# Kernel tuning notes

Measured on AMD Instinct MI355X. Metric: run time of the kernel, lower is better.

Reference implementation:

```python
import jax, jax.numpy as jnp
import numpy as np

DIM = 1024
HEADS = 16
DIM_HEAD = 64
INNER = HEADS * DIM_HEAD
SCALE = DIM_HEAD ** -0.5


def setup_inputs() -> dict:
    key = jax.random.key(0)
    ks = jax.random.split(key, 9)
    B, N = 4, 4096
    x = jax.random.normal(ks[0], (B, N, DIM), dtype=jnp.float32)
    mask = jnp.ones((B, N), dtype=bool)
    s = 0.02
    W_qkv = jax.random.normal(ks[1], (DIM, INNER * 3), dtype=jnp.float32) * s
    w_q = jax.random.normal(ks[2], (DIM_HEAD,), dtype=jnp.float32) * s
    w_k = jax.random.normal(ks[3], (DIM_HEAD,), dtype=jnp.float32) * s
    W_r = jax.random.normal(ks[4], (DIM_HEAD, DIM_HEAD), dtype=jnp.float32) * s
    b_r = jnp.zeros((DIM_HEAD,), dtype=jnp.float32)
    W_out = jax.random.normal(ks[5], (INNER, DIM), dtype=jnp.float32) * s
    b_out = jnp.zeros((DIM,), dtype=jnp.float32)
    return {"x": x, "mask": mask, "W_qkv": W_qkv, "w_q": w_q, "w_k": w_k,
            "W_r": W_r, "b_r": b_r, "W_out": W_out, "b_out": b_out}


def reference(x, mask, W_qkv, w_q, w_k, W_r, b_r, W_out, b_out):
    B, N, D = x.shape
    h, dh = HEADS, DIM_HEAD
    mask_value = -jnp.finfo(x.dtype).max

    qkv = x @ W_qkv                                  # [B,N,3*inner]
    q, k, v = jnp.split(qkv, 3, axis=-1)
    tohead = lambda t: t.reshape(B, N, h, dh).transpose(0, 2, 1, 3)  # b h n d
    q, k, v = tohead(q), tohead(k), tohead(v)
    m = mask[:, None, :]                             # b 1 n

    # global query via softmax-pooled per-token logits
    q_logits = jnp.einsum('bhnd,d->bhn', q, w_q) * SCALE
    q_attn = jax.nn.softmax(jnp.where(m, q_logits, mask_value), axis=-1)
    global_q = jnp.einsum('bhn,bhnd->bhd', q_attn, q)[:, :, None, :]  # b h 1 d

    k = k * global_q
    k_logits = jnp.einsum('bhnd,d->bhn', k, w_k) * SCALE
    k_attn = jax.nn.softmax(jnp.where(m, k_logits, mask_value), axis=-1)
    global_k = jnp.einsum('bhn,bhnd->bhd', k_attn, k)[:, :, None, :]  # b h 1 d

    v = v * global_k
    r = jnp.einsum('bhnd,de->bhne', v, W_r) + b_r + q  # to_r(v) + q
    r = r.transpose(0, 2, 1, 3).reshape(B, N, h * dh)  # b n (h d)
    return r @ W_out + b_out
```

## Files before the change

kernel.cpp:

```cpp
#include <hip/hip_runtime.h>
#include <hip/hip_bf16.h>
#include <math.h>

#define B_    4
#define N_    4096
#define D_    1024
#define H_    16
#define DH_   64
#define M_TOT (B_ * N_)
#define QKV3  (3 * D_)
#define SCALE_ 0.125f
#define NSPLIT 16

typedef float f32x4 __attribute__((ext_vector_type(4)));
typedef __bf16 bf16x8 __attribute__((ext_vector_type(8)));
typedef unsigned short u16;
typedef unsigned int u32;

__device__ __forceinline__ float bf2f(u16 u) {
    union { u32 i; float f; } v; v.i = ((u32)u) << 16; return v.f;
}
__device__ __forceinline__ u16 f2bf(float f) {
    union { float f; u32 i; } v; v.f = f;
    u32 r = (v.i + 0x7fffu + ((v.i >> 16) & 1u)) >> 16;
    return (u16)r;
}

__global__ __launch_bounds__(256) void prep(const float* __restrict__ x, u16* __restrict__ xb,
                                            const float* __restrict__ Wqkv, u16* __restrict__ wqkv,
                                            const float* __restrict__ Wout, u16* __restrict__ wout) {
    __shared__ float t[32][33];
    const int bid = blockIdx.x, tid = threadIdx.x;
    if (bid < 16384) {
        const int i = bid * 256 + tid;
        float4 v = ((const float4*)x)[i];
        ushort4 o;
        o.x = f2bf(v.x); o.y = f2bf(v.y); o.z = f2bf(v.z); o.w = f2bf(v.w);
        ((ushort4*)xb)[i] = o;
        return;
    }
    const float* in; u16* out; int K, N, bx, by;
    if (bid < 16384 + 3072) {
        const int b2 = bid - 16384;
        in = Wqkv; out = wqkv; K = D_; N = QKV3; bx = b2 % 96; by = b2 / 96;
    } else {
        const int b2 = bid - 19456;
        in = Wout; out = wout; K = D_; N = D_; bx = b2 & 31; by = b2 >> 5;
    }
    const int n0 = bx * 32, k0 = by * 32;
    const int tx = tid & 31, ty = tid >> 5;
#pragma unroll
    for (int r = 0; r < 32; r += 8)
        t[ty + r][tx] = in[(size_t)(k0 + ty + r) * N + n0 + tx];
    __syncthreads();
#pragma unroll
    for (int r = 0; r < 32; r += 8)
        out[(size_t)(n0 + ty + r) * K + k0 + tx] = f2bf(t[tx][ty + r]);
}

#define BM 256
#define BN 256
#define BK 32

template <bool SCATTER, bool SWIZ>
__global__ __launch_bounds__(512, 2) void gemm_bt(const u16* __restrict__ A,
                                                  const u16* __restrict__ Bt,
                                                  void* __restrict__ Cout,
                                                  const float* __restrict__ bias,
                                                  int M, int N, int K) {
    __shared__ u16 lds[65536];
    const int tid = threadIdx.x;
    const int lane = tid & 63, wave = tid >> 6;
    const int wm = wave >> 2, wn = wave & 3;
    u32 bx = blockIdx.x, by = blockIdx.y;
    if (SWIZ) {
        const u32 nwg = gridDim.x * gridDim.y;
        const u32 lid = by * gridDim.x + bx;
        const u32 chunk = nwg >> 3;
        const u32 nid = (lid & 7) * chunk + (lid >> 3);
        bx = nid % gridDim.x; by = nid / gridDim.x;
    }
    const int m0 = by * BM, n0 = bx * BN;

    const int srow = tid >> 2;
    const int scol = 8 * ((tid & 3) ^ ((tid >> 3) & 3));
    const u16* aSrc = A + (size_t)(m0 + srow) * K + scol;
    const u16* bSrc = Bt + (size_t)(n0 + srow) * K + scol;
    const u32 dOff = (u32)wave * 512u;

    const int cbu = 8 * ((lane >> 4) ^ ((lane >> 1) & 3));
    const u32 arow = (u32)(wm * 128 + (lane & 15)) * 32u + cbu;
    const u32 brow = 32768u + (u32)(wn * 64 + (lane & 15)) * 32u + cbu;

    f32x4 acc[8][4] = {};

#define GLOAD(src, off) __builtin_amdgcn_global_load_lds(                          \
        (__attribute__((address_space(1))) const void*)(src),                      \
        (__attribute__((address_space(3))) void*)&lds[off], 16, 0, 0)
#define STAGE(t) { const size_t ko = (size_t)(t) * BK; const u32 sb_ = ((t) & 3) * 8192u; \
        GLOAD(aSrc + ko,                   sb_ + dOff);                            \
        GLOAD(aSrc + ko + (size_t)128 * K, sb_ + 4096u + dOff);                    \
        GLOAD(bSrc + ko,                   32768u + sb_ + dOff);                   \
        GLOAD(bSrc + ko + (size_t)128 * K, 32768u + sb_ + 4096u + dOff); }

    const int NT = K >> 5;
    STAGE(0); STAGE(1); STAGE(2);

    for (int t = 0; t < NT; ++t) {
        if (t + 3 <= NT)      asm volatile("s_waitcnt vmcnt(8)" ::: "memory");
        else if (t + 2 == NT) asm volatile("s_waitcnt vmcnt(4)" ::: "memory");
        else                  asm volatile("s_waitcnt vmcnt(0)" ::: "memory");
        __builtin_amdgcn_s_barrier();
        if (t + 3 < NT) STAGE(t + 3);

        const u32 sb = (u32)(t & 3) * 8192u;
        bf16x8 af[8], bfr[4];
#pragma unroll
        for (int i = 0; i < 8; i++) af[i] = *(const bf16x8*)&lds[sb + arow + i * 512];
#pragma unroll
        for (int j = 0; j < 4; j++) bfr[j] = *(const bf16x8*)&lds[sb + brow + j * 512];
        __builtin_amdgcn_s_setprio(1);
#pragma unroll
        for (int i = 0; i < 8; i++)
#pragma unroll
            for (int j = 0; j < 4; j++)
                acc[i][j] = __builtin_amdgcn_mfma_f32_16x16x32_bf16(af[i], bfr[j], acc[i][j], 0, 0, 0);
        __builtin_amdgcn_s_setprio(0);
    }
#undef STAGE
#undef GLOAD

    __syncthreads();
    const int cr = (lane >> 4) * 4;
    const int cc = lane & 15;
    u16* reg = &lds[(u32)wave * 8192u];

    if (SCATTER) {
#pragma unroll
        for (int i = 0; i < 8; i++)
#pragma unroll
            for (int j = 0; j < 4; j++)
#pragma unroll
                for (int r = 0; r < 4; r++)
                    reg[(i * 16 + cr + r) * 64 + j * 16 + cc] = f2bf(acc[i][j][r]);
        const int colb = n0 + wn * 64;
        const int part = colb >> 10, hh = (colb >> 6) & (H_ - 1);
        const int grow0 = m0 + wm * 128;
        const int bb = grow0 >> 12, nn0 = grow0 & (N_ - 1);
        u16* plane = (u16*)Cout + (((size_t)(part * B_ + bb) * H_ + hh) * N_) * DH_;
        const int lr8 = lane >> 3, le = (lane & 7) * 8;
#pragma unroll
        for (int p = 0; p < 16; p++) {
            const int lr = p * 8 + lr8;
            const uint4 w = *(const uint4*)&reg[lr * 64 + le];
            *(uint4*)(plane + (size_t)(nn0 + lr) * DH_ + le) = w;
        }
    } else {
        float* regf = (float*)reg;
        const int lr4 = lane >> 4, le4 = (lane & 15) * 4;
        float bv[4];
#pragma unroll
        for (int j = 0; j < 4; j++)
            bv[j] = bias ? bias[n0 + wn * 64 + j * 16 + cc] : 0.f;
#pragma unroll
        for (int h = 0; h < 2; h++) {
#pragma unroll
            for (int i2 = 0; i2 < 4; i2++) {
                const int i = h * 4 + i2;
#pragma unroll
                for (int j = 0; j < 4; j++)
#pragma unroll
                    for (int r = 0; r < 4; r++)
                        regf[(i2 * 16 + cr + r) * 64 + j * 16 + cc] = acc[i][j][r] + bv[j];
            }
#pragma unroll
            for (int p = 0; p < 16; p++) {
                const int lr = p * 4 + lr4;
                const float4 w = *(const float4*)&regf[lr * 64 + le4];
                *(float4*)((float*)Cout + (size_t)(m0 + wm * 128 + h * 64 + lr) * N
                           + n0 + wn * 64 + le4) = w;
            }
            if (!h) __syncthreads();
        }
    }
}

template <bool KPHASE>
__global__ __launch_bounds__(256) void pool_partial(const u16* __restrict__ plane,
                                                    const float* __restrict__ wvec,
                                                    const float* __restrict__ partq,
                                                    float* __restrict__ part) {
    __shared__ float sm[32], sl[32], sacc[32][64];
    __shared__ float gqsh[64];
    const int bh = blockIdx.x, s = blockIdx.y;
    const int tid = threadIdx.x;
    const int sub = tid >> 3, j = tid & 7;
    const size_t base = (size_t)bh * N_ * DH_ + (size_t)s * (N_ / NSPLIT) * DH_ + j * 8;

    if (KPHASE) {
        if (tid < 64) {
            float M = -INFINITY;
            for (int t = 0; t < NSPLIT; t++) M = fmaxf(M, partq[((size_t)bh * NSPLIT + t) * 66]);
            float L = 0.f, ssum = 0.f;
            for (int t = 0; t < NSPLIT; t++) {
                const float* o = partq + ((size_t)bh * NSPLIT + t) * 66;
                const float e = __expf(o[0] - M);
                L += o[1] * e;
                ssum += o[2 + tid] * e;
            }
            gqsh[tid] = ssum / L;
        }
        __syncthreads();
    }

    float wv[8], gq[8];
#pragma unroll
    for (int i = 0; i < 8; i++) wv[i] = wvec[j * 8 + i];
    if (KPHASE) {
#pragma unroll
        for (int i = 0; i < 8; i++) gq[i] = gqsh[j * 8 + i];
    }

    float m = -INFINITY, l = 0.f, acc[8];
#pragma unroll
    for (int i = 0; i < 8; i++) acc[i] = 0.f;
    const int ITER = N_ / NSPLIT / 32;
    uint4 raw = *(const uint4*)(plane + base + (size_t)sub * DH_);
    for (int it = 0; it < ITER; it++) {
        uint4 nxt;
        if (it + 1 < ITER)
            nxt = *(const uint4*)(plane + base + (size_t)((it + 1) * 32 + sub) * DH_);
        const u16* pu = (const u16*)&raw;
        float f[8], p = 0.f;
#pragma unroll
        for (int i = 0; i < 8; i++) {
            f[i] = bf2f(pu[i]);
            if (KPHASE) f[i] *= gq[i];
            p += f[i] * wv[i];
        }
        p += __shfl_xor(p, 1); p += __shfl_xor(p, 2); p += __shfl_xor(p, 4);
        p *= SCALE_;
        const float mn = fmaxf(m, p);
        const float sc = __expf(m - mn);
        const float w = __expf(p - mn);
        m = mn; l = l * sc + w;
#pragma unroll
        for (int i = 0; i < 8; i++) acc[i] = acc[i] * sc + w * f[i];
        raw = nxt;
    }
    if (j == 0) { sm[sub] = m; sl[sub] = l; }
#pragma unroll
    for (int i = 0; i < 8; i++) sacc[sub][j * 8 + i] = acc[i];
    __syncthreads();
    if (tid < 64) {
        float M = -INFINITY;
        for (int g = 0; g < 32; g++) M = fmaxf(M, sm[g]);
        float L = 0.f, ssum = 0.f;
        for (int g = 0; g < 32; g++) {
            const float e = __expf(sm[g] - M);
            L += sl[g] * e;
            ssum += sacc[g][tid] * e;
        }
        float* o = part + ((size_t)bh * NSPLIT + s) * 66;
        if (tid == 0) { o[0] = M; o[1] = L; }
        o[2 + tid] = ssum;
    }
}

__global__ __launch_bounds__(256) void apply_r_mfma(const u16* __restrict__ qkv,
                                                    const float* __restrict__ Wr,
                                                    const float* __restrict__ br,
                                                    const float* __restrict__ partk,
                                                    u16* __restrict__ rout) {
    __shared__ u16 Mt[64][136];
    __shared__ float gksh[64];
    __shared__ u16 rb[4][64 * 64];
    const int bh = blockIdx.y;
    const int b = bh >> 4, h = bh & 15;
    const int tid = threadIdx.x, lane = tid & 63, wave = tid >> 6;

    if (tid < 64) {
        float M = -INFINITY;
        for (int t = 0; t < NSPLIT; t++) M = fmaxf(M, partk[((size_t)bh * NSPLIT + t) * 66]);
        float L = 0.f, ssum = 0.f;
        for (int t = 0; t < NSPLIT; t++) {
            const float* o = partk + ((size_t)bh * NSPLIT + t) * 66;
            const float e = __expf(o[0] - M);
            L += o[1] * e;
            ssum += o[2 + tid] * e;
        }
        gksh[tid] = ssum / L;
    }
    __syncthreads();

    for (int idx = tid; idx < 4096; idx += 256) {
        const int d = idx >> 6, e = idx & 63;
        Mt[e][d] = f2bf(gksh[d] * Wr[idx]);
        Mt[e][64 + d] = (d == e) ? (u16)0x3F80 : (u16)0;
    }
    __syncthreads();

    const size_t qbase = (size_t)bh * N_ * DH_;
    const size_t vbase = (size_t)(2 * B_ * H_ + bh) * N_ * DH_;
    const int row0 = blockIdx.x * 256 + wave * 64;
    const int fr = lane & 15;
    const int fk8 = (lane >> 4) * 8;
    f32x4 acc[4][4] = {};

#pragma unroll
    for (int ks = 0; ks < 4; ks++) {
        const int kd = ks * 32 + fk8;
        bf16x8 af[4], bf[4];
#pragma unroll
        for (int i = 0; i < 4; i++) {
            const int row = row0 + i * 16 + fr;
            const size_t off = (kd < 64) ? (vbase + (size_t)row * DH_ + kd)
                                         : (qbase + (size_t)row * DH_ + (kd - 64));
            af[i] = *(const bf16x8*)(qkv + off);
        }
#pragma unroll
        for (int j = 0; j < 4; j++)
            bf[j] = *(const bf16x8*)&Mt[j * 16 + fr][kd];
#pragma unroll
        for (int i = 0; i < 4; i++)
#pragma unroll
            for (int j = 0; j < 4; j++)
                acc[i][j] = __builtin_amdgcn_mfma_f32_16x16x32_bf16(af[i], bf[j], acc[i][j], 0, 0, 0);
    }

    const int cr = (lane >> 4) * 4;
    const int cc = lane & 15;
#pragma unroll
    for (int j = 0; j < 4; j++) {
        const float bv = br[j * 16 + cc];
#pragma unroll
        for (int i = 0; i < 4; i++)
#pragma unroll
            for (int r = 0; r < 4; r++)
                rb[wave][(i * 16 + cr + r) * 64 + j * 16 + cc] = f2bf(acc[i][j][r] + bv);
    }
    const int lr8 = lane >> 3, le = (lane & 7) * 8;
#pragma unroll
    for (int p = 0; p < 8; p++) {
        const int lr = p * 8 + lr8;
        const uint4 w = *(const uint4*)&rb[wave][lr * 64 + le];
        *(uint4*)(rout + (size_t)(b * N_ + row0 + lr) * D_ + h * DH_ + le) = w;
    }
}

extern "C" void kernel_launch(void* const* d_in, const int* in_sizes, int n_in,
                              void* d_out, int out_size, void* d_ws, size_t ws_size,
                              hipStream_t stream) {
    const float* x = (const float*)d_in[0];
    const float* W_qkv = (const float*)d_in[2];
    const float* w_q = (const float*)d_in[3];
    const float* w_k = (const float*)d_in[4];
    const float* W_r = (const float*)d_in[5];
    const float* b_r = (const float*)d_in[6];
    const float* W_out = (const float*)d_in[7];
    const float* b_out = (const float*)d_in[8];
    float* out = (float*)d_out;

    u16* xb = (u16*)d_ws;
    u16* wqkv = xb + (size_t)M_TOT * D_;
    u16* wout = wqkv + (size_t)QKV3 * D_;
    u16* qkv = wout + (size_t)D_ * D_;
    u16* rbuf = qkv + (size_t)M_TOT * QKV3;
    float* partq = (float*)(rbuf + (size_t)M_TOT * D_);
    float* partk = partq + 64 * NSPLIT * 66;

    prep<<<16384 + 3072 + 1024, 256, 0, stream>>>(x, xb, W_qkv, wqkv, W_out, wout);

    gemm_bt<true, true><<<dim3(QKV3 / BN, M_TOT / BM), 512, 0, stream>>>(
        xb, wqkv, qkv, nullptr, M_TOT, QKV3, D_);

    pool_partial<false><<<dim3(64, NSPLIT), 256, 0, stream>>>(qkv, w_q, nullptr, partq);
    pool_partial<true><<<dim3(64, NSPLIT), 256, 0, stream>>>(
        qkv + (size_t)(B_ * H_) * N_ * DH_, w_k, partq, partk);

    apply_r_mfma<<<dim3(N_ / 256, 64), 256, 0, stream>>>(qkv, W_r, b_r, partk, rbuf);

    gemm_bt<false, true><<<dim3(D_ / BN, M_TOT / BM), 512, 0, stream>>>(
        rbuf, wout, out, b_out, M_TOT, D_, D_);
}
```

Before: 331.9 us.

## Fuse pooling and apply kernels into one persistent kernel with grid barriers

Merges the two pooling passes and the r-projection kernel into a single 512-block kernel that synchronises through atomic grid-wide barriers, and halves the pooling split count so the block count fits co-residency. The prep kernel now has each block convert 8 float4s of x instead of one, cutting its block count, and it resets the barrier counters. This removes two kernel launch gaps and their tail effects. The cost is spin-waiting at the barriers, a deadlock risk if not all 512 blocks are resident at once, and fewer pooling blocks doing more sequential work each.

```diff
diff --git a/kernel.cpp b/kernel.cpp
--- a/kernel.cpp
+++ b/kernel.cpp
@@ -10,7 +10,7 @@
 #define M_TOT (B_ * N_)
 #define QKV3  (3 * D_)
 #define SCALE_ 0.125f
-#define NSPLIT 16
+#define NSPLIT 8
 
 typedef float f32x4 __attribute__((ext_vector_type(4)));
 typedef __bf16 bf16x8 __attribute__((ext_vector_type(8)));
@@ -28,23 +28,29 @@
 
 __global__ __launch_bounds__(256) void prep(const float* __restrict__ x, u16* __restrict__ xb,
                                             const float* __restrict__ Wqkv, u16* __restrict__ wqkv,
-                                            const float* __restrict__ Wout, u16* __restrict__ wout) {
+                                            const float* __restrict__ Wout, u16* __restrict__ wout,
+                                            u32* __restrict__ bar) {
     __shared__ float t[32][33];
     const int bid = blockIdx.x, tid = threadIdx.x;
-    if (bid < 16384) {
-        const int i = bid * 256 + tid;
-        float4 v = ((const float4*)x)[i];
-        ushort4 o;
-        o.x = f2bf(v.x); o.y = f2bf(v.y); o.z = f2bf(v.z); o.w = f2bf(v.w);
-        ((ushort4*)xb)[i] = o;
+    if (bid < 2048) {
+        if (bid == 0 && tid == 0) { bar[0] = 0u; bar[1] = 0u; }
+        const int base = bid * 2048 + tid;
+#pragma unroll
+        for (int k = 0; k < 8; k++) {
+            const int i = base + k * 256;
+            float4 v = ((const float4*)x)[i];
+            ushort4 o;
+            o.x = f2bf(v.x); o.y = f2bf(v.y); o.z = f2bf(v.z); o.w = f2bf(v.w);
+            ((ushort4*)xb)[i] = o;
+        }
         return;
     }
     const float* in; u16* out; int K, N, bx, by;
-    if (bid < 16384 + 3072) {
-        const int b2 = bid - 16384;
+    if (bid < 2048 + 3072) {
+        const int b2 = bid - 2048;
         in = Wqkv; out = wqkv; K = D_; N = QKV3; bx = b2 % 96; by = b2 / 96;
     } else {
-        const int b2 = bid - 19456;
+        const int b2 = bid - 5120;
         in = Wout; out = wout; K = D_; N = D_; bx = b2 & 31; by = b2 >> 5;
     }
     const int n0 = bx * 32, k0 = by * 32;
@@ -185,14 +191,25 @@
     }
 }
 
+__device__ __forceinline__ void gridbar(u32* c, u32 target) {
+    __syncthreads();
+    if (threadIdx.x == 0) {
+        __threadfence();
+        __hip_atomic_fetch_add(c, 1u, __ATOMIC_ACQ_REL, __HIP_MEMORY_SCOPE_AGENT);
+        while (__hip_atomic_load(c, __ATOMIC_ACQUIRE, __HIP_MEMORY_SCOPE_AGENT) < target)
+            __builtin_amdgcn_s_sleep(8);
+    }
+    __syncthreads();
+}
+
 template <bool KPHASE>
-__global__ __launch_bounds__(256) void pool_partial(const u16* __restrict__ plane,
-                                                    const float* __restrict__ wvec,
-                                                    const float* __restrict__ partq,
-                                                    float* __restrict__ part) {
-    __shared__ float sm[32], sl[32], sacc[32][64];
-    __shared__ float gqsh[64];
-    const int bh = blockIdx.x, s = blockIdx.y;
+__device__ __forceinline__ void pool_body(const u16* __restrict__ plane,
+                                          const float* __restrict__ wvec,
+                                          const float* __restrict__ partq,
+                                          float* __restrict__ part,
+                                          int bh, int s,
+                                          float* sm, float* sl, float (*sacc)[64],
+                                          float* gqsh) {
     const int tid = threadIdx.x;
     const int sub = tid >> 3, j = tid & 7;
     const size_t base = (size_t)bh * N_ * DH_ + (size_t)s * (N_ / NSPLIT) * DH_ + j * 8;
@@ -265,19 +282,35 @@
         if (tid == 0) { o[0] = M; o[1] = L; }
         o[2 + tid] = ssum;
     }
-}
-
-__global__ __launch_bounds__(256) void apply_r_mfma(const u16* __restrict__ qkv,
-                                                    const float* __restrict__ Wr,
-                                                    const float* __restrict__ br,
-                                                    const float* __restrict__ partk,
-                                                    u16* __restrict__ rout) {
-    __shared__ u16 Mt[64][136];
-    __shared__ float gksh[64];
-    __shared__ u16 rb[4][64 * 64];
-    const int bh = blockIdx.y;
+    __syncthreads();
+}
+
+__global__ __launch_bounds__(256) void pool_apply(const u16* __restrict__ qkv,
+                                                  const float* __restrict__ wq,
+                                                  const float* __restrict__ wk,
+                                                  const float* __restrict__ Wr,
+                                                  const float* __restrict__ br,
+                                                  float* __restrict__ partq,
+                                                  float* __restrict__ partk,
+                                                  u16* __restrict__ rout,
+                                                  u32* __restrict__ bar) {
+    __shared__ union {
+        struct { float sm[32], sl[32], sacc[32][64], gqsh[64]; } p;
+        struct { u16 Mt[64][136]; float gksh[64]; u16 rb[4][64 * 64]; } a;
+    } sh;
+    const int blk = blockIdx.x, tid = threadIdx.x;
+    const int lane = tid & 63, wave = tid >> 6;
+
+    pool_body<false>(qkv, wq, nullptr, partq, blk >> 3, blk & 7,
+                     sh.p.sm, sh.p.sl, sh.p.sacc, sh.p.gqsh);
+    gridbar(&bar[0], 512);
+
+    pool_body<true>(qkv + (size_t)(B_ * H_) * N_ * DH_, wk, partq, partk, blk >> 3, blk & 7,
+                    sh.p.sm, sh.p.sl, sh.p.sacc, sh.p.gqsh);
+    gridbar(&bar[1], 512);
+
+    const int bh = blk >> 3;
     const int b = bh >> 4, h = bh & 15;
-    const int tid = threadIdx.x, lane = tid & 63, wave = tid >> 6;
 
     if (tid < 64) {
         float M = -INFINITY;
@@ -289,62 +322,66 @@
             L += o[1] * e;
             ssum += o[2 + tid] * e;
         }
-        gksh[tid] = ssum / L;
+        sh.a.gksh[tid] = ssum / L;
     }
     __syncthreads();
 
     for (int idx = tid; idx < 4096; idx += 256) {
         const int d = idx >> 6, e = idx & 63;
-        Mt[e][d] = f2bf(gksh[d] * Wr[idx]);
-        Mt[e][64 + d] = (d == e) ? (u16)0x3F80 : (u16)0;
+        sh.a.Mt[e][d] = f2bf(sh.a.gksh[d] * Wr[idx]);
+        sh.a.Mt[e][64 + d] = (d == e) ? (u16)0x3F80 : (u16)0;
     }
     __syncthreads();
 
     const size_t qbase = (size_t)bh * N_ * DH_;
     const size_t vbase = (size_t)(2 * B_ * H_ + bh) * N_ * DH_;
-    const int row0 = blockIdx.x * 256 + wave * 64;
     const int fr = lane & 15;
     const int fk8 = (lane >> 4) * 8;
-    f32x4 acc[4][4] = {};
-
-#pragma unroll
-    for (int ks = 0; ks < 4; ks++) {
-        const int kd = ks * 32 + fk8;
-        bf16x8 af[4], bf[4];
-#pragma unroll
-        for (int i = 0; i < 4; i++) {
-            const int row = row0 + i * 16 + fr;
-            const size_t off = (kd < 64) ? (vbase + (size_t)row * DH_ + kd)
-                                         : (qbase + (size_t)row * DH_ + (kd - 64));
-            af[i] = *(const bf16x8*)(qkv + off);
-        }
-#pragma unroll
-        for (int j = 0; j < 4; j++)
-            bf[j] = *(const bf16x8*)&Mt[j * 16 + fr][kd];
-#pragma unroll
-        for (int i = 0; i < 4; i++)
-#pragma unroll
-            for (int j = 0; j < 4; j++)
-                acc[i][j] = __builtin_amdgcn_mfma_f32_16x16x32_bf16(af[i], bf[j], acc[i][j], 0, 0, 0);
-    }
-
     const int cr = (lane >> 4) * 4;
     const int cc = lane & 15;
-#pragma unroll
-    for (int j = 0; j < 4; j++) {
-        const float bv = br[j * 16 + cc];
-#pragma unroll
-        for (int i = 0; i < 4; i++)
-#pragma unroll
-            for (int r = 0; r < 4; r++)
-                rb[wave][(i * 16 + cr + r) * 64 + j * 16 + cc] = f2bf(acc[i][j][r] + bv);
-    }
     const int lr8 = lane >> 3, le = (lane & 7) * 8;
-#pragma unroll
-    for (int p = 0; p < 8; p++) {
-        const int lr = p * 8 + lr8;
-        const uint4 w = *(const uint4*)&rb[wave][lr * 64 + le];
-        *(uint4*)(rout + (size_t)(b * N_ + row0 + lr) * D_ + h * DH_ + le) = w;
+
+    for (int u = 0; u < 2; u++) {
+        const int bx = ((blk & 7) << 1) | u;
+        const int row0 = bx * 256 + wave * 64;
+        f32x4 acc[4][4] = {};
+
+#pragma unroll
+        for (int ks = 0; ks < 4; ks++) {
+            const int kd = ks * 32 + fk8;
+            bf16x8 af[4], bf[4];
+#pragma unroll
+            for (int i = 0; i < 4; i++) {
+                const int row = row0 + i * 16 + fr;
+                const size_t off = (kd < 64) ? (vbase + (size_t)row * DH_ + kd)
+                                             : (qbase + (size_t)row * DH_ + (kd - 64));
+                af[i] = *(const bf16x8*)(qkv + off);
+            }
+#pragma unroll
+            for (int j = 0; j < 4; j++)
+                bf[j] = *(const bf16x8*)&sh.a.Mt[j * 16 + fr][kd];
+#pragma unroll
+            for (int i = 0; i < 4; i++)
+#pragma unroll
+                for (int j = 0; j < 4; j++)
+                    acc[i][j] = __builtin_amdgcn_mfma_f32_16x16x32_bf16(af[i], bf[j], acc[i][j], 0, 0, 0);
+        }
+
+#pragma unroll
+        for (int j = 0; j < 4; j++) {
+            const float bv = br[j * 16 + cc];
+#pragma unroll
+            for (int i = 0; i < 4; i++)
+#pragma unroll
+                for (int r = 0; r < 4; r++)
+                    sh.a.rb[wave][(i * 16 + cr + r) * 64 + j * 16 + cc] = f2bf(acc[i][j][r] + bv);
+        }
+#pragma unroll
+        for (int p = 0; p < 8; p++) {
+            const int lr = p * 8 + lr8;
+            const uint4 w = *(const uint4*)&sh.a.rb[wave][lr * 64 + le];
+            *(uint4*)(rout + (size_t)(b * N_ + row0 + lr) * D_ + h * DH_ + le) = w;
+        }
     }
 }
 
@@ -368,17 +405,14 @@
     u16* rbuf = qkv + (size_t)M_TOT * QKV3;
     float* partq = (float*)(rbuf + (size_t)M_TOT * D_);
     float* partk = partq + 64 * NSPLIT * 66;
-
-    prep<<<16384 + 3072 + 1024, 256, 0, stream>>>(x, xb, W_qkv, wqkv, W_out, wout);
+    u32* bar = (u32*)(partk + 64 * NSPLIT * 66);
+
+    prep<<<6144, 256, 0, stream>>>(x, xb, W_qkv, wqkv, W_out, wout, bar);
 
     gemm_bt<true, true><<<dim3(QKV3 / BN, M_TOT / BM), 512, 0, stream>>>(
         xb, wqkv, qkv, nullptr, M_TOT, QKV3, D_);
 
-    pool_partial<false><<<dim3(64, NSPLIT), 256, 0, stream>>>(qkv, w_q, nullptr, partq);
-    pool_partial<true><<<dim3(64, NSPLIT), 256, 0, stream>>>(
-        qkv + (size_t)(B_ * H_) * N_ * DH_, w_k, partq, partk);
-
-    apply_r_mfma<<<dim3(N_ / 256, 64), 256, 0, stream>>>(qkv, W_r, b_r, partk, rbuf);
+    pool_apply<<<512, 256, 0, stream>>>(qkv, w_q, w_k, W_r, b_r, partq, partk, rbuf, bar);
 
     gemm_bt<false, true><<<dim3(D_ / BN, M_TOT / BM), 512, 0, stream>>>(
         rbuf, wout, out, b_out, M_TOT, D_, D_);
```

Result: slower. 361.6 us (+8.9%).
